# Kernel optimization log

Hardware: AMD Instinct MI355X
Metric: run time of the kernel (lower is better)

## Reference

```python
import jax, jax.numpy as jnp
import numpy as np

EPS = 1e-8


def setup_inputs() -> dict:
    key = jax.random.key(0)
    ks = jax.random.split(key, 10)
    B, Cin, H, W = 16, 256, 64, 64
    D, C = 128, 32
    return {
        "f_curr": jax.random.normal(ks[0], (B, Cin, H, W), jnp.float32),
        "mu_prior": jax.random.normal(ks[1], (B, D, C), jnp.float32),
        "log_sigma_prior": jax.random.normal(ks[2], (B, D, C), jnp.float32),
        "pi_prior": jax.random.uniform(ks[3], (B, C), jnp.float32),
        "mu_post": jax.random.normal(ks[4], (B, D), jnp.float32),
        "log_sigma_post": jax.random.normal(ks[5], (B, D), jnp.float32),
        "noise_cluster": jax.random.normal(ks[6], (B, D), jnp.float32),
        "noise_z": jax.random.normal(ks[7], (B, D), jnp.float32),
        "proj_W": jax.random.normal(ks[8], (Cin, Cin + D), jnp.float32) * 0.02,
        "proj_b": jax.random.normal(ks[9], (Cin,), jnp.float32) * 0.02,
    }


def reference(f_curr, mu_prior, log_sigma_prior, pi_prior, mu_post,
              log_sigma_post, noise_cluster, noise_z, proj_W, proj_b):
    sg = jax.lax.stop_gradient

    # ---- _cluster_sampler (all stats detached in the original) ----
    mu_p, ls_p = sg(mu_post), sg(log_sigma_post)          # [B, D]
    mu_pr, ls_pr = sg(mu_prior), sg(log_sigma_prior)      # [B, D, C]
    z_post = mu_p + jnp.exp(ls_p) * noise_cluster          # Normal(mu, exp(ls)).sample()
    sigma_pr = jnp.exp(ls_pr)
    # Normal log_prob of z_post[:, :, None] under each cluster -> [B, D, C]
    log_probs = (-ls_pr - 0.5 * jnp.log(2.0 * jnp.pi)
                 - (z_post[:, :, None] - mu_pr) ** 2 / (2.0 * sigma_pr ** 2))
    log_prob_c = jnp.sum(log_probs, axis=1)                # [B, C]
    pi_post = jax.nn.softmax(log_prob_c, axis=1)           # [B, C]

    # ---- z_c = Normal(mu_post, exp(ls)+eps).sample()  (no grad: .sample()) ----
    z_c = sg(mu_post + (jnp.exp(log_sigma_post) + EPS) * noise_z)  # [B, D]

    # ---- _f_combine: concat + 1x1 conv, computed as split matmuls ----
    Cin = f_curr.shape[1]
    Wf, Wz = proj_W[:, :Cin], proj_W[:, Cin:]              # [Cin,Cin], [Cin,D]
    bias = jnp.einsum('bd,od->bo', z_c, Wz) + proj_b       # spatially-constant part
    f_out = jnp.einsum('bchw,oc->bohw', f_curr, Wf) + bias[:, :, None, None]

    # ---- _kld ----
    mu_post_e = mu_post[:, :, None]                        # [B, D, 1]
    ls_post_e = log_sigma_post[:, :, None]
    sigma_prior = jnp.exp(log_sigma_prior)
    sigma_post = jnp.exp(ls_post_e)
    kl_g = (log_sigma_prior - ls_post_e
            + (sigma_post ** 2 + (mu_post_e - mu_prior) ** 2)
            / (2.0 * sigma_prior ** 2 + EPS) - 0.5)
    kl_g = jnp.sum(kl_g, axis=1)                           # [B, C]
    kl_g_weighted = jnp.sum(pi_post * kl_g, axis=1)        # [B]
    kl_cat = jnp.sum(pi_post * (jnp.log(pi_post + EPS) - jnp.log(pi_prior + EPS)), axis=1)  # [B]
    kl_std = jnp.sum(-ls_post_e + 0.5 * (jnp.exp(2.0 * ls_post_e) + mu_post_e ** 2) - 0.5,
                     axis=1)                               # [B, 1]
    # NOTE: original torch code broadcasts [B] + [B,1] -> [B,B] before mean; replicated here.
    kld = jnp.mean((kl_g_weighted + kl_cat) + kl_std)

    return f_out, kld
```

## Files before the change

kernel.cpp:

```cpp
#include <hip/hip_runtime.h>
#include <math.h>

#define EPS_F 1e-8f

typedef __attribute__((ext_vector_type(8))) short bf16x8;
typedef __attribute__((ext_vector_type(4))) float f32x4;

__device__ inline short f2bf(float f) {
    union { float f; unsigned u; } v; v.f = f;
    unsigned r = (v.u + 0x7fffu + ((v.u >> 16) & 1u)) >> 16;
    return (short)r;
}

__global__ __launch_bounds__(256) void prelim_kernel(
    const float* __restrict__ mu_prior,
    const float* __restrict__ ls_prior,
    const float* __restrict__ pi_prior,
    const float* __restrict__ mu_post,
    const float* __restrict__ ls_post,
    const float* __restrict__ noise_c,
    const float* __restrict__ noise_z,
    const float* __restrict__ projW,
    const float* __restrict__ projb,
    float* __restrict__ ws_bias,
    float* __restrict__ kld_out)
{
    const int b = blockIdx.x;
    const int t = threadIdx.x;

    __shared__ float s_zpost[128];
    __shared__ float s_zc[128];
    __shared__ float s_mu[128];
    __shared__ float s_e2[128];
    __shared__ float s_lsp[128];
    __shared__ float s_kstd[128];
    __shared__ float s_p1[8][32];
    __shared__ float s_p2[8][32];

    if (t < 128) {
        const float mu = mu_post[b * 128 + t];
        const float ls = ls_post[b * 128 + t];
        const float el = __expf(ls);
        s_zpost[t] = mu + el * noise_c[b * 128 + t];
        s_zc[t]    = mu + (el + EPS_F) * noise_z[b * 128 + t];
        s_mu[t]    = mu;
        s_e2[t]    = el * el;
        s_lsp[t]   = ls;
        s_kstd[t]  = -ls + 0.5f * (el * el + mu * mu) - 0.5f;
    }
    __syncthreads();

    {
        const int c = t & 31;
        const int g = t >> 5;
        const float* mpB = mu_prior + b * 4096;
        const float* lpB = ls_prior + b * 4096;
        float lp = 0.f, kg = 0.f;
#pragma unroll 4
        for (int j = 0; j < 16; ++j) {
            const int d = g * 16 + j;
            const float mpr  = mpB[d * 32 + c];
            const float lpr  = lpB[d * 32 + c];
            const float inv2 = 0.5f * __expf(-2.f * lpr);
            const float zd   = s_zpost[d] - mpr;
            lp += -lpr - 0.91893853320467274f - zd * zd * inv2;
            const float dm   = s_mu[d] - mpr;
            const float e2pr = __expf(2.f * lpr);
            kg += lpr - s_lsp[d]
                + (s_e2[d] + dm * dm) * __builtin_amdgcn_rcpf(2.f * e2pr + EPS_F)
                - 0.5f;
        }
        s_p1[g][c] = lp;
        s_p2[g][c] = kg;
    }
    __syncthreads();

    if (t < 64) {
        const int c = t & 31;
        float lp = 0.f, kg = 0.f;
#pragma unroll
        for (int g = 0; g < 8; ++g) { lp += s_p1[g][c]; kg += s_p2[g][c]; }
        float ks = s_kstd[c] + s_kstd[c + 32] + s_kstd[c + 64] + s_kstd[c + 96];
        const float pp = pi_prior[b * 32 + c];

        float m = lp;
#pragma unroll
        for (int o = 16; o; o >>= 1) m = fmaxf(m, __shfl_xor(m, o, 32));
        const float e = __expf(lp - m);
        float den = e;
#pragma unroll
        for (int o = 16; o; o >>= 1) den += __shfl_xor(den, o, 32);
        const float pi = e * __builtin_amdgcn_rcpf(den);
        float tot = pi * kg + pi * (__logf(pi + EPS_F) - __logf(pp + EPS_F));
#pragma unroll
        for (int o = 16; o; o >>= 1) tot += __shfl_xor(tot, o, 32);
#pragma unroll
        for (int o = 16; o; o >>= 1) ks += __shfl_xor(ks, o, 32);
        if (t == 0) atomicAdd(kld_out, (tot + ks) * 0.0625f);
    }

    {
        const int o = t;
        const float4* wrow = (const float4*)(projW + o * 384 + 256);
        float sum = projb[o];
#pragma unroll 8
        for (int j = 0; j < 32; ++j) {
            const float4 w = wrow[j];
            sum += s_zc[4 * j + 0] * w.x + s_zc[4 * j + 1] * w.y +
                   s_zc[4 * j + 2] * w.z + s_zc[4 * j + 3] * w.w;
        }
        ws_bias[b * 256 + o] = sum;
    }
}

__global__ __launch_bounds__(256) void gemm_kernel(
    const float* __restrict__ F,
    const float* __restrict__ W,
    const float* __restrict__ bias,
    float* __restrict__ O)
{
    const int nT = blockIdx.x;
    const int oT = blockIdx.y;
    const int b  = blockIdx.z;

    __shared__ short A_lds[4][128][8];
    __shared__ short B_lds[4][128][8];
    __shared__ float s_bias[128];

    const int tid  = threadIdx.x;
    const int lane = tid & 63;
    const int wave = tid >> 6;
    const int wm = wave & 1;
    const int wn = wave >> 1;

    const float* Fb = F + (size_t)b * 256 * 4096 + (size_t)nT * 128;

    const int sbn  = tid & 127;
    const int sbkg = (tid >> 7) * 2;
    const int sao  = tid >> 1;
    const int sakg = (tid & 1) * 2;

    if (tid < 128) s_bias[tid] = bias[b * 256 + oT * 128 + tid];

    const float* bptr = Fb + (size_t)(sbkg * 8) * 4096 + sbn;
    const float* aptr = W + (size_t)(oT * 128 + sao) * 384 + sakg * 8;

    float fb[16];
    float4 fa0, fa1, fa2, fa3;

#pragma unroll
    for (int i = 0; i < 16; ++i) fb[i] = bptr[(size_t)i * 4096];
    fa0 = *(const float4*)(aptr);
    fa1 = *(const float4*)(aptr + 4);
    fa2 = *(const float4*)(aptr + 8);
    fa3 = *(const float4*)(aptr + 12);

    f32x4 acc[4][4];
#pragma unroll
    for (int i = 0; i < 4; ++i)
#pragma unroll
        for (int j = 0; j < 4; ++j) acc[i][j] = (f32x4){0.f, 0.f, 0.f, 0.f};

    const int kg = lane >> 4;
    const int lm = lane & 15;

    for (int kc = 0; kc < 8; ++kc) {
        bf16x8 vb0, vb1, va0, va1;
#pragma unroll
        for (int i = 0; i < 8; ++i) vb0[i] = f2bf(fb[i]);
#pragma unroll
        for (int i = 0; i < 8; ++i) vb1[i] = f2bf(fb[8 + i]);
        va0[0] = f2bf(fa0.x); va0[1] = f2bf(fa0.y); va0[2] = f2bf(fa0.z); va0[3] = f2bf(fa0.w);
        va0[4] = f2bf(fa1.x); va0[5] = f2bf(fa1.y); va0[6] = f2bf(fa1.z); va0[7] = f2bf(fa1.w);
        va1[0] = f2bf(fa2.x); va1[1] = f2bf(fa2.y); va1[2] = f2bf(fa2.z); va1[3] = f2bf(fa2.w);
        va1[4] = f2bf(fa3.x); va1[5] = f2bf(fa3.y); va1[6] = f2bf(fa3.z); va1[7] = f2bf(fa3.w);

        __syncthreads();
        *(bf16x8*)&B_lds[sbkg][sbn][0]      = vb0;
        *(bf16x8*)&B_lds[sbkg + 1][sbn][0]  = vb1;
        *(bf16x8*)&A_lds[sakg][sao][0]      = va0;
        *(bf16x8*)&A_lds[sakg + 1][sao][0]  = va1;
        __syncthreads();

        if (kc < 7) {
            const float* bp = bptr + (size_t)(kc + 1) * 32 * 4096;
#pragma unroll
            for (int i = 0; i < 16; ++i) fb[i] = bp[(size_t)i * 4096];
            const float* ap = aptr + (kc + 1) * 32;
            fa0 = *(const float4*)(ap);
            fa1 = *(const float4*)(ap + 4);
            fa2 = *(const float4*)(ap + 8);
            fa3 = *(const float4*)(ap + 12);
        }

        bf16x8 aF[4], bF[4];
#pragma unroll
        for (int mt = 0; mt < 4; ++mt)
            aF[mt] = *(const bf16x8*)&A_lds[kg][wm * 64 + mt * 16 + lm][0];
#pragma unroll
        for (int nt = 0; nt < 4; ++nt)
            bF[nt] = *(const bf16x8*)&B_lds[kg][wn * 64 + nt * 16 + lm][0];

#pragma unroll
        for (int mt = 0; mt < 4; ++mt)
#pragma unroll
            for (int nt = 0; nt < 4; ++nt)
                acc[mt][nt] = __builtin_amdgcn_mfma_f32_16x16x32_bf16(
                    aF[mt], bF[nt], acc[mt][nt], 0, 0, 0);
    }

    float* Ob = O + (size_t)b * 256 * 4096 + (size_t)oT * 128 * 4096;
    const int rbase = wm * 64 + (lane >> 4) * 4;
    const int cbase = nT * 128 + wn * 64 + lm;
#pragma unroll
    for (int mt = 0; mt < 4; ++mt) {
#pragma unroll
        for (int r = 0; r < 4; ++r) {
            const int row = rbase + mt * 16 + r;
            const float bb = s_bias[row];
            float* orow = Ob + (size_t)row * 4096 + cbase;
#pragma unroll
            for (int nt = 0; nt < 4; ++nt)
                orow[nt * 16] = acc[mt][nt][r] + bb;
        }
    }
}

extern "C" void kernel_launch(void* const* d_in, const int* in_sizes, int n_in,
                              void* d_out, int out_size, void* d_ws, size_t ws_size,
                              hipStream_t stream) {
    const float* f_curr   = (const float*)d_in[0];
    const float* mu_prior = (const float*)d_in[1];
    const float* ls_prior = (const float*)d_in[2];
    const float* pi_prior = (const float*)d_in[3];
    const float* mu_post  = (const float*)d_in[4];
    const float* ls_post  = (const float*)d_in[5];
    const float* noise_c  = (const float*)d_in[6];
    const float* noise_z  = (const float*)d_in[7];
    const float* projW    = (const float*)d_in[8];
    const float* projb    = (const float*)d_in[9];

    float* out = (float*)d_out;
    float* ws  = (float*)d_ws;
    float* ws_bias = ws;

    float* kld_out = out + 16777216;
    hipMemsetAsync(kld_out, 0, sizeof(float), stream);

    prelim_kernel<<<16, 256, 0, stream>>>(mu_prior, ls_prior, pi_prior, mu_post,
                                          ls_post, noise_c, noise_z, projW, projb,
                                          ws_bias, kld_out);
    gemm_kernel<<<dim3(32, 2, 16), 256, 0, stream>>>(f_curr, projW, ws_bias, out);
}
```

Before: 158.0 us.

## Pre-convert weights to bf16 fragment layout and load MFMA operands directly from global

The prelim kernel now converts the Wf weight block to bf16 and writes it to workspace in the MFMA fragment layout. The GEMM then reads A fragments straight from global memory. B fragments are loaded per lane from f_curr into a double-buffered register array and converted in registers. This removes the LDS staging and the two barriers per k-step. The cost is that each wave independently reloads B and A with no sharing through LDS, so global and L2 traffic rise. The strided 4096-float loads per lane may also coalesce poorly, and the register footprint grows.

```diff
diff --git a/kernel.cpp b/kernel.cpp
--- a/kernel.cpp
+++ b/kernel.cpp
@@ -23,10 +23,22 @@
     const float* __restrict__ projW,
     const float* __restrict__ projb,
     float* __restrict__ ws_bias,
+    short* __restrict__ ws_A,
     float* __restrict__ kld_out)
 {
     const int b = blockIdx.x;
     const int t = threadIdx.x;
+
+    {
+        const float* wrow = projW + t * 384 + b * 16;
+        bf16x8 w0, w1;
+#pragma unroll
+        for (int j = 0; j < 8; ++j) w0[j] = f2bf(wrow[j]);
+#pragma unroll
+        for (int j = 0; j < 8; ++j) w1[j] = f2bf(wrow[8 + j]);
+        *(bf16x8*)&ws_A[(b * 2 + 0) * 2048 + t * 8] = w0;
+        *(bf16x8*)&ws_A[(b * 2 + 1) * 2048 + t * 8] = w1;
+    }
 
     __shared__ float s_zpost[128];
     __shared__ float s_zc[128];
@@ -115,7 +127,7 @@
 
 __global__ __launch_bounds__(256) void gemm_kernel(
     const float* __restrict__ F,
-    const float* __restrict__ W,
+    const short* __restrict__ wsA,
     const float* __restrict__ bias,
     float* __restrict__ O)
 {
@@ -123,8 +135,6 @@
     const int oT = blockIdx.y;
     const int b  = blockIdx.z;
 
-    __shared__ short A_lds[4][128][8];
-    __shared__ short B_lds[4][128][8];
     __shared__ float s_bias[128];
 
     const int tid  = threadIdx.x;
@@ -132,74 +142,53 @@
     const int wave = tid >> 6;
     const int wm = wave & 1;
     const int wn = wave >> 1;
-
-    const float* Fb = F + (size_t)b * 256 * 4096 + (size_t)nT * 128;
-
-    const int sbn  = tid & 127;
-    const int sbkg = (tid >> 7) * 2;
-    const int sao  = tid >> 1;
-    const int sakg = (tid & 1) * 2;
-
-    if (tid < 128) s_bias[tid] = bias[b * 256 + oT * 128 + tid];
-
-    const float* bptr = Fb + (size_t)(sbkg * 8) * 4096 + sbn;
-    const float* aptr = W + (size_t)(oT * 128 + sao) * 384 + sakg * 8;
-
-    float fb[16];
-    float4 fa0, fa1, fa2, fa3;
-
-#pragma unroll
-    for (int i = 0; i < 16; ++i) fb[i] = bptr[(size_t)i * 4096];
-    fa0 = *(const float4*)(aptr);
-    fa1 = *(const float4*)(aptr + 4);
-    fa2 = *(const float4*)(aptr + 8);
-    fa3 = *(const float4*)(aptr + 12);
-
-    f32x4 acc[4][4];
-#pragma unroll
-    for (int i = 0; i < 4; ++i)
-#pragma unroll
-        for (int j = 0; j < 4; ++j) acc[i][j] = (f32x4){0.f, 0.f, 0.f, 0.f};
-
     const int kg = lane >> 4;
     const int lm = lane & 15;
 
+    if (tid < 128) s_bias[tid] = bias[b * 256 + oT * 128 + tid];
+
+    const short* aBase = wsA + (size_t)kg * 2048 + (oT * 128 + wm * 64 + lm) * 8;
+    const float* bBase = F + (size_t)b * 1048576 + (size_t)(kg * 8) * 4096
+                       + nT * 128 + wn * 64 + lm;
+
+    f32x4 acc[4][4];
+#pragma unroll
+    for (int i = 0; i < 4; ++i)
+#pragma unroll
+        for (int j = 0; j < 4; ++j) acc[i][j] = (f32x4){0.f, 0.f, 0.f, 0.f};
+
+    float Bbuf[2][32];
+
+#pragma unroll
+    for (int nt = 0; nt < 4; ++nt)
+#pragma unroll
+        for (int j = 0; j < 8; ++j)
+            Bbuf[0][nt * 8 + j] = bBase[(size_t)j * 4096 + nt * 16];
+
+#pragma unroll
     for (int kc = 0; kc < 8; ++kc) {
-        bf16x8 vb0, vb1, va0, va1;
-#pragma unroll
-        for (int i = 0; i < 8; ++i) vb0[i] = f2bf(fb[i]);
-#pragma unroll
-        for (int i = 0; i < 8; ++i) vb1[i] = f2bf(fb[8 + i]);
-        va0[0] = f2bf(fa0.x); va0[1] = f2bf(fa0.y); va0[2] = f2bf(fa0.z); va0[3] = f2bf(fa0.w);
-        va0[4] = f2bf(fa1.x); va0[5] = f2bf(fa1.y); va0[6] = f2bf(fa1.z); va0[7] = f2bf(fa1.w);
-        va1[0] = f2bf(fa2.x); va1[1] = f2bf(fa2.y); va1[2] = f2bf(fa2.z); va1[3] = f2bf(fa2.w);
-        va1[4] = f2bf(fa3.x); va1[5] = f2bf(fa3.y); va1[6] = f2bf(fa3.z); va1[7] = f2bf(fa3.w);
-
-        __syncthreads();
-        *(bf16x8*)&B_lds[sbkg][sbn][0]      = vb0;
-        *(bf16x8*)&B_lds[sbkg + 1][sbn][0]  = vb1;
-        *(bf16x8*)&A_lds[sakg][sao][0]      = va0;
-        *(bf16x8*)&A_lds[sakg + 1][sao][0]  = va1;
-        __syncthreads();
+        const int cur = kc & 1, nxt = cur ^ 1;
 
         if (kc < 7) {
-            const float* bp = bptr + (size_t)(kc + 1) * 32 * 4096;
-#pragma unroll
-            for (int i = 0; i < 16; ++i) fb[i] = bp[(size_t)i * 4096];
-            const float* ap = aptr + (kc + 1) * 32;
-            fa0 = *(const float4*)(ap);
-            fa1 = *(const float4*)(ap + 4);
-            fa2 = *(const float4*)(ap + 8);
-            fa3 = *(const float4*)(ap + 12);
-        }
-
-        bf16x8 aF[4], bF[4];
+            const float* bp = bBase + (size_t)(kc + 1) * 32 * 4096;
+#pragma unroll
+            for (int nt = 0; nt < 4; ++nt)
+#pragma unroll
+                for (int j = 0; j < 8; ++j)
+                    Bbuf[nxt][nt * 8 + j] = bp[(size_t)j * 4096 + nt * 16];
+        }
+
+        bf16x8 aF[4];
 #pragma unroll
         for (int mt = 0; mt < 4; ++mt)
-            aF[mt] = *(const bf16x8*)&A_lds[kg][wm * 64 + mt * 16 + lm][0];
+            aF[mt] = *(const bf16x8*)(aBase + (size_t)kc * 8192 + mt * 128);
+
+        bf16x8 bF[4];
 #pragma unroll
         for (int nt = 0; nt < 4; ++nt)
-            bF[nt] = *(const bf16x8*)&B_lds[kg][wn * 64 + nt * 16 + lm][0];
+#pragma unroll
+            for (int j = 0; j < 8; ++j)
+                bF[nt][j] = f2bf(Bbuf[cur][nt * 8 + j]);
 
 #pragma unroll
         for (int mt = 0; mt < 4; ++mt)
@@ -209,8 +198,10 @@
                     aF[mt], bF[nt], acc[mt][nt], 0, 0, 0);
     }
 
-    float* Ob = O + (size_t)b * 256 * 4096 + (size_t)oT * 128 * 4096;
-    const int rbase = wm * 64 + (lane >> 4) * 4;
+    __syncthreads();
+
+    float* Ob = O + (size_t)b * 1048576 + (size_t)oT * 128 * 4096;
+    const int rbase = wm * 64 + kg * 4;
     const int cbase = nT * 128 + wn * 64 + lm;
 #pragma unroll
     for (int mt = 0; mt < 4; ++mt) {
@@ -243,12 +234,13 @@
     float* out = (float*)d_out;
     float* ws  = (float*)d_ws;
     float* ws_bias = ws;
+    short* ws_A    = (short*)(ws + 4096);
 
     float* kld_out = out + 16777216;
     hipMemsetAsync(kld_out, 0, sizeof(float), stream);
 
     prelim_kernel<<<16, 256, 0, stream>>>(mu_prior, ls_prior, pi_prior, mu_post,
                                           ls_post, noise_c, noise_z, projW, projb,
-                                          ws_bias, kld_out);
-    gemm_kernel<<<dim3(32, 2, 16), 256, 0, stream>>>(f_curr, projW, ws_bias, out);
-}
+                                          ws_bias, ws_A, kld_out);
+    gemm_kernel<<<dim3(32, 2, 16), 256, 0, stream>>>(f_curr, ws_A, ws_bias, out);
+}
```

New measurement: 164.7 us. 4.2% more time.
